# Kernel optimization log

Measured on AMD Instinct MI355X. Metric: run time of the kernel, lower is better.

## Reference

```python
import jax, jax.numpy as jnp
import numpy as np

# --- hyperparameters (from MambaBlock init) ---
DIM = 256          # d_model per window
STEP = 128         # int(dim * hop), hop = 0.5
N_MAMBA = 2
D_STATE = 16
D_CONV = 4
EXPAND = 4
D_INNER = EXPAND * DIM          # 1024
DT_RANK = -(-DIM // 16)         # ceil(d_model/16) = 16
EPS = 1e-5
B_SZ = 4
T_LEN = 131072


def setup_inputs() -> dict:
    key = jax.random.key(0)
    ks = jax.random.split(key, 8)
    s = 0.02
    x = jax.random.normal(ks[0], (B_SZ, T_LEN), dtype=jnp.float32)
    in_proj_w = jax.random.normal(ks[1], (N_MAMBA, 2 * D_INNER, DIM), dtype=jnp.float32) * s
    conv_w = jax.random.normal(ks[2], (N_MAMBA, D_INNER, 1, D_CONV), dtype=jnp.float32) * 0.1
    conv_b = jnp.zeros((N_MAMBA, D_INNER), dtype=jnp.float32)
    x_proj_w = jax.random.normal(ks[3], (N_MAMBA, DT_RANK + 2 * D_STATE, D_INNER), dtype=jnp.float32) * s
    dt_std = DT_RANK ** -0.5
    dt_proj_w = jax.random.uniform(ks[4], (N_MAMBA, D_INNER, DT_RANK), minval=-dt_std, maxval=dt_std, dtype=jnp.float32)
    # dt bias: inverse-softplus of dt ~ LogUniform[1e-3, 0.1] (mamba_ssm init)
    dt = jnp.exp(jax.random.uniform(ks[5], (N_MAMBA, D_INNER), dtype=jnp.float32)
                 * (np.log(0.1) - np.log(1e-3)) + np.log(1e-3))
    dt_proj_b = dt + jnp.log(-jnp.expm1(-dt))
    A_log = jnp.log(jnp.broadcast_to(jnp.arange(1, D_STATE + 1, dtype=jnp.float32),
                                     (N_MAMBA, D_INNER, D_STATE)))
    D_param = jnp.ones((N_MAMBA, D_INNER), dtype=jnp.float32)
    out_proj_w = jax.random.normal(ks[6], (N_MAMBA, DIM, D_INNER), dtype=jnp.float32) * s
    norm_w = jnp.ones((N_MAMBA, DIM), dtype=jnp.float32)
    return dict(x=x, in_proj_w=in_proj_w, conv_w=conv_w, conv_b=conv_b,
                x_proj_w=x_proj_w, dt_proj_w=dt_proj_w, dt_proj_b=dt_proj_b,
                A_log=A_log, D_param=D_param, out_proj_w=out_proj_w, norm_w=norm_w)


def _rmsnorm(x, w):
    return x * jax.lax.rsqrt(jnp.mean(x * x, axis=-1, keepdims=True) + EPS) * w


def _selective_scan(u, delta, A, Bm, Cm, Dp):
    # u, delta: [B, L, Di]; A: [Di, N]; Bm, Cm: [B, L, N]; Dp: [Di]
    def step(h, inp):
        u_t, d_t, B_t, C_t = inp                       # [B,Di],[B,Di],[B,N],[B,N]
        dA = jnp.exp(d_t[:, :, None] * A)              # [B,Di,N]
        h = dA * h + (d_t * u_t)[:, :, None] * B_t[:, None, :]
        y_t = jnp.einsum('bdn,bn->bd', h, C_t)
        return h, y_t
    h0 = jnp.zeros((u.shape[0], u.shape[2], A.shape[1]), u.dtype)
    xs = (u.transpose(1, 0, 2), delta.transpose(1, 0, 2),
          Bm.transpose(1, 0, 2), Cm.transpose(1, 0, 2))
    _, ys = jax.lax.scan(step, h0, xs)                 # ys: [L, B, Di]
    return ys.transpose(1, 0, 2) + u * Dp


def _mamba(x, in_w, cw, cb, xp_w, dt_w, dt_b, A_log, Dp, out_w):
    # x: [B, L, d_model]
    xz = jnp.einsum('bld,ed->ble', x, in_w)            # [B, L, 2*Di]
    xc, z = jnp.split(xz, 2, axis=-1)
    # causal depthwise conv (torch pads d_conv-1 both sides then truncates to L)
    xc = xc.transpose(0, 2, 1)                         # [B, Di, L]
    xc = jax.lax.conv_general_dilated(xc, cw, window_strides=(1,),
                                      padding=[(D_CONV - 1, 0)],
                                      feature_group_count=D_INNER,
                                      dimension_numbers=('NCH', 'OIH', 'NCH'))
    xc = jax.nn.silu(xc + cb[None, :, None]).transpose(0, 2, 1)  # [B, L, Di]
    x_dbl = jnp.einsum('bld,ed->ble', xc, xp_w)        # [B, L, dt_rank + 2N]
    dt = x_dbl[..., :DT_RANK]
    Bm = x_dbl[..., DT_RANK:DT_RANK + D_STATE]
    Cm = x_dbl[..., DT_RANK + D_STATE:]
    delta = jax.nn.softplus(jnp.einsum('blr,dr->bld', dt, dt_w) + dt_b)
    A = -jnp.exp(A_log)                                # [Di, N]
    y = _selective_scan(xc, delta, A, Bm, Cm, Dp)
    y = y * jax.nn.silu(z)
    return jnp.einsum('bld,ed->ble', y, out_w)         # [B, L, d_model]


def _forward(x, in_proj_w, conv_w, conv_b, x_proj_w, dt_proj_w, dt_proj_b,
             A_log, D_param, out_proj_w, norm_w):
    B, T = x.shape
    L = (T - DIM) // STEP + 1
    idx = jnp.arange(L)[:, None] * STEP + jnp.arange(DIM)[None, :]  # [L, DIM]
    h = x[:, idx]                                      # unfold -> [B, L, DIM]
    res = None
    for i in range(N_MAMBA):
        res = h + res if res is not None else h        # Block residual chaining
        hn = _rmsnorm(res, norm_w[i])
        h = _mamba(hn, in_proj_w[i], conv_w[i], conv_b[i], x_proj_w[i],
                   dt_proj_w[i], dt_proj_b[i], A_log[i], D_param[i], out_proj_w[i])
    r = h + res
    # hop < 1: triangular window, then fold (overlap-add)
    half = DIM // 2
    win = jnp.concatenate([jnp.linspace(0.0, 1.0, half), jnp.linspace(1.0, 0.0, half)])
    r = r * win
    folded = jnp.zeros_like(x).at[:, idx].add(r)       # F.fold overlap-add
    return folded + x


def reference(x, in_proj_w, conv_w, conv_b, x_proj_w, dt_proj_w, dt_proj_b,
              A_log, D_param, out_proj_w, norm_w):
    return _forward(x, in_proj_w, conv_w, conv_b, x_proj_w, dt_proj_w, dt_proj_b,
                    A_log, D_param, out_proj_w, norm_w)
```

## Files before the change

kernel.cpp:

```cpp
#include <hip/hip_runtime.h>
#include <cmath>

#define DIMC   256
#define L_WIN  1023
#define M_VALID 4092
#define M_PAD  4096
#define DI     1024
#define TLEN   131072
#define SEG    64
#define NSEG   16
#define CBT    8

typedef __bf16 bf16x8 __attribute__((ext_vector_type(8)));
typedef __bf16 bf16x4 __attribute__((ext_vector_type(4)));
typedef float  f32x4  __attribute__((ext_vector_type(4)));

#define LOG2E 1.4426950408889634f

__device__ __forceinline__ float sigmoidf_(float x){ return 1.f/(1.f + __expf(-x)); }
__device__ __forceinline__ float softplusf_(float v){ return fmaxf(v,0.f) + log1pf(__expf(-fabsf(v))); }

template<int CTRL>
__device__ __forceinline__ float dpp_add(float x){
  int v = __builtin_amdgcn_update_dpp(0, __builtin_bit_cast(int, x), CTRL, 0xF, 0xF, true);
  return x + __builtin_bit_cast(float, v);
}

__global__ __launch_bounds__(256) void init_kernel(const float* __restrict__ x, float* __restrict__ res,
    __bf16* __restrict__ hn16, const float* __restrict__ w0,
    const float* __restrict__ a, __bf16* __restrict__ da, int na,
    const float* __restrict__ b, __bf16* __restrict__ db, int nb,
    const float* __restrict__ c, __bf16* __restrict__ dc, int nc)
{
  if (blockIdx.x < M_PAD){
    int m = blockIdx.x, j = threadIdx.x;
    float v = 0.f;
    if (m < M_VALID){
      int bb = m / L_WIN, l = m - bb*L_WIN;
      v = x[(size_t)bb*TLEN + l*128 + j];
    }
    res[(size_t)m*DIMC + j] = v;
    float s = v*v;
    #pragma unroll
    for (int off = 32; off; off >>= 1) s += __shfl_down(s, off);
    __shared__ float ls[4];
    if ((threadIdx.x & 63) == 0) ls[threadIdx.x >> 6] = s;
    __syncthreads();
    float tot = ls[0] + ls[1] + ls[2] + ls[3];
    float scale = rsqrtf(tot * (1.f/DIMC) + 1e-5f);
    hn16[(size_t)m*DIMC + j] = (__bf16)(v * scale * w0[j]);
    return;
  }
  int nblk = gridDim.x - M_PAD;
  int stride = nblk*256;
  int base = (blockIdx.x - M_PAD)*256 + threadIdx.x;
  for (int i = base; i < na; i += stride) da[i] = (__bf16)a[i];
  for (int i = base; i < nb; i += stride) db[i] = (__bf16)b[i];
  for (int i = base; i < nc; i += stride) dc[i] = (__bf16)c[i];
}

__global__ __launch_bounds__(256) void rms_kernel(const float* __restrict__ src, __bf16* __restrict__ dst,
                                                  const float* __restrict__ w){
  int m = blockIdx.x, j = threadIdx.x;
  float v = (m < M_VALID) ? src[(size_t)m*DIMC + j] : 0.f;
  float s = v*v;
  #pragma unroll
  for (int off = 32; off; off >>= 1) s += __shfl_down(s, off);
  __shared__ float ls[4];
  if ((threadIdx.x & 63) == 0) ls[threadIdx.x >> 6] = s;
  __syncthreads();
  float tot = ls[0] + ls[1] + ls[2] + ls[3];
  float scale = rsqrtf(tot * (1.f/DIMC) + 1e-5f);
  dst[(size_t)m*DIMC + j] = (__bf16)(v * scale * w[j]);
}

template<int WM, int WN, typename OutT>
__global__ __launch_bounds__(256) void gemm_tiled_kernel(const __bf16* __restrict__ A, const __bf16* __restrict__ B,
    OutT* C, const float* addsrc, int K, int ldc)
{
  constexpr int BM  = 32*WM;
  constexpr int BN  = 32*WN;
  constexpr int LDK = 72;
  __shared__ __bf16 As[BM*LDK];
  __shared__ __bf16 Bs[BN*LDK];
  int tid  = threadIdx.x;
  int lane = tid & 63, wv = tid >> 6;
  int row  = lane & 15, kq = lane >> 4;
  int m0 = blockIdx.x*BM, n0 = blockIdx.y*BN;
  int wmo = (wv >> 1)*(16*WM);
  int wno = (wv &  1)*(16*WN);
  f32x4 acc[WM][WN] = {};
  for (int kt = 0; kt < K; kt += 64){
    __syncthreads();
    #pragma unroll
    for (int r = 0; r < BM/32; ++r){
      int seg = r*256 + tid;
      int rw = seg >> 3, sb = seg & 7;
      *(bf16x8*)(As + rw*LDK + sb*8) = *(const bf16x8*)(A + (size_t)(m0 + rw)*K + kt + sb*8);
    }
    #pragma unroll
    for (int r = 0; r < BN/32; ++r){
      int seg = r*256 + tid;
      int rw = seg >> 3, sb = seg & 7;
      *(bf16x8*)(Bs + rw*LDK + sb*8) = *(const bf16x8*)(B + (size_t)(n0 + rw)*K + kt + sb*8);
    }
    __syncthreads();
    #pragma unroll
    for (int ks = 0; ks < 2; ++ks){
      bf16x8 af[WM], bfr[WN];
      #pragma unroll
      for (int i = 0; i < WM; ++i) af[i]  = *(const bf16x8*)(As + (wmo + i*16 + row)*LDK + ks*32 + kq*8);
      #pragma unroll
      for (int j = 0; j < WN; ++j) bfr[j] = *(const bf16x8*)(Bs + (wno + j*16 + row)*LDK + ks*32 + kq*8);
      #pragma unroll
      for (int i = 0; i < WM; ++i){
        #pragma unroll
        for (int j = 0; j < WN; ++j)
          acc[i][j] = __builtin_amdgcn_mfma_f32_16x16x32_bf16(af[i], bfr[j], acc[i][j], 0, 0, 0);
      }
    }
  }
  #pragma unroll
  for (int i = 0; i < WM; ++i){
    int cm = m0 + wmo + i*16 + kq*4;
    #pragma unroll
    for (int j = 0; j < WN; ++j){
      int cn = n0 + wno + j*16 + row;
      #pragma unroll
      for (int ii = 0; ii < 4; ++ii){
        size_t idx = (size_t)(cm + ii)*ldc + cn;
        float v = acc[i][j][ii];
        if (addsrc) v += addsrc[idx];
        C[idx] = (OutT)v;
      }
    }
  }
}

__global__ __launch_bounds__(256) void conv_xproj_dt_kernel(
  const __bf16* __restrict__ xz16, const float* __restrict__ cw, const float* __restrict__ cb,
  const __bf16* __restrict__ wxp, const float* __restrict__ dtw, const float* __restrict__ dtb,
  __bf16* __restrict__ u16, float* __restrict__ xdbl, __bf16* __restrict__ delta16)
{
  __shared__ __bf16 su[16][1032];
  __shared__ float  sdt[CBT][17];
  __shared__ f32x4  spart[4][3][64];
  int tid = threadIdx.x;
  int m0 = blockIdx.x * CBT;
  {
    int d = tid * 4;
    float w[4][4], bias[4];
    #pragma unroll
    for (int c = 0; c < 4; ++c){
      #pragma unroll
      for (int j = 0; j < 4; ++j) w[c][j] = cw[(d + c)*4 + j];
      bias[c] = cb[d + c];
    }
    bf16x4 zero4; zero4[0] = (__bf16)0.f; zero4[1] = (__bf16)0.f; zero4[2] = (__bf16)0.f; zero4[3] = (__bf16)0.f;
    bf16x4 rm3 = (m0 >= 3) ? *(const bf16x4*)(xz16 + (size_t)(m0-3)*2048 + d) : zero4;
    bf16x4 rm2 = (m0 >= 2) ? *(const bf16x4*)(xz16 + (size_t)(m0-2)*2048 + d) : zero4;
    bf16x4 rm1 = (m0 >= 1) ? *(const bf16x4*)(xz16 + (size_t)(m0-1)*2048 + d) : zero4;
    for (int ti = 0; ti < CBT; ++ti){
      int m = m0 + ti;
      bf16x4 cur = *(const bf16x4*)(xz16 + (size_t)m*2048 + d);
      float acc[4] = {0.f, 0.f, 0.f, 0.f};
      if (m < M_VALID){
        int b = m / L_WIN;
        int l = m - b*L_WIN;
        #pragma unroll
        for (int c = 0; c < 4; ++c) acc[c] = fmaf((float)cur[c], w[c][3], bias[c]);
        if (l >= 1){
          #pragma unroll
          for (int c = 0; c < 4; ++c) acc[c] = fmaf((float)rm1[c], w[c][2], acc[c]);
        }
        if (l >= 2){
          #pragma unroll
          for (int c = 0; c < 4; ++c) acc[c] = fmaf((float)rm2[c], w[c][1], acc[c]);
        }
        if (l >= 3){
          #pragma unroll
          for (int c = 0; c < 4; ++c) acc[c] = fmaf((float)rm3[c], w[c][0], acc[c]);
        }
        #pragma unroll
        for (int c = 0; c < 4; ++c) acc[c] = acc[c] * sigmoidf_(acc[c]);
      }
      bf16x4 o;
      #pragma unroll
      for (int c = 0; c < 4; ++c) o[c] = (__bf16)acc[c];
      *(bf16x4*)(u16 + (size_t)m*DI + d) = o;
      *(bf16x4*)(&su[ti][d]) = o;
      rm3 = rm2; rm2 = rm1; rm1 = cur;
    }
  }
  __syncthreads();
  {
    int lane = tid & 63, wv = tid >> 6;
    int row = lane & 15, kq = lane >> 4;
    int kbase = wv * 256;
    f32x4 acc0 = {0,0,0,0}, acc1 = {0,0,0,0}, acc2 = {0,0,0,0};
    const __bf16* B0 = wxp + (size_t)(row)*1024      + kbase + kq*8;
    const __bf16* B1 = wxp + (size_t)(16 + row)*1024 + kbase + kq*8;
    const __bf16* B2 = wxp + (size_t)(32 + row)*1024 + kbase + kq*8;
    #pragma unroll
    for (int k = 0; k < 256; k += 32){
      bf16x8 a = *(const bf16x8*)(&su[row][kbase + k + kq*8]);
      acc0 = __builtin_amdgcn_mfma_f32_16x16x32_bf16(a, *(const bf16x8*)(B0 + k), acc0, 0, 0, 0);
      acc1 = __builtin_amdgcn_mfma_f32_16x16x32_bf16(a, *(const bf16x8*)(B1 + k), acc1, 0, 0, 0);
      acc2 = __builtin_amdgcn_mfma_f32_16x16x32_bf16(a, *(const bf16x8*)(B2 + k), acc2, 0, 0, 0);
    }
    spart[wv][0][lane] = acc0;
    spart[wv][1][lane] = acc1;
    spart[wv][2][lane] = acc2;
  }
  __syncthreads();
  if (tid < 192){
    int tno = tid >> 6, lane = tid & 63;
    int row = lane & 15, kq = lane >> 4;
    f32x4 sum = spart[0][tno][lane];
    sum += spart[1][tno][lane];
    sum += spart[2][tno][lane];
    sum += spart[3][tno][lane];
    #pragma unroll
    for (int i = 0; i < 4; ++i){
      int tok = kq*4 + i;
      if (tok < CBT){
        xdbl[(size_t)(m0 + tok)*48 + tno*16 + row] = sum[i];
        if (tno == 0) sdt[tok][row] = sum[i];
      }
    }
  }
  __syncthreads();
  {
    int d0 = tid * 4;
    float w[4][16], bias[4];
    #pragma unroll
    for (int c = 0; c < 4; ++c){
      #pragma unroll
      for (int q = 0; q < 16; ++q) w[c][q] = dtw[(d0 + c)*16 + q];
      bias[c] = dtb[d0 + c];
    }
    for (int t = 0; t < CBT; ++t){
      float acc[4] = {bias[0], bias[1], bias[2], bias[3]};
      #pragma unroll
      for (int r = 0; r < 16; ++r){
        float dv = sdt[t][r];
        #pragma unroll
        for (int c = 0; c < 4; ++c) acc[c] = fmaf(dv, w[c][r], acc[c]);
      }
      bf16x4 o;
      #pragma unroll
      for (int c = 0; c < 4; ++c) o[c] = (__bf16)softplusf_(acc[c]);
      *(bf16x4*)(delta16 + (size_t)(m0 + t)*DI + d0) = o;
    }
  }
}

__global__ __launch_bounds__(256) void scan_part1_kernel(
  const __bf16* __restrict__ u16, const __bf16* __restrict__ delta16,
  const float* __restrict__ xdbl, const float* __restrict__ Alog, float2* __restrict__ Pq)
{
  int bid = blockIdx.x;
  int s = bid & 15, dtile = (bid >> 4) & 63, b = bid >> 10;
  if (s == 15) return;
  int d0 = dtile << 4;
  int tid = threadIdx.x;
  int c = tid >> 4, n = tid & 15;
  float A2 = -__expf(Alog[(d0 + c)*16 + n]) * LOG2E;
  __shared__ float2 sdd[16][SEG+2];
  __shared__ float  sB [SEG][17];
  int t0 = s*SEG;
  int nt = L_WIN - t0; if (nt > SEG) nt = SEG;
  size_t base_m = (size_t)b*L_WIN + t0;
  if (tid < 128){
    int row = tid >> 1, half = tid & 1;
    bf16x8 dl8, u8;
    if (row < nt){
      size_t m = base_m + row;
      dl8 = *(const bf16x8*)(delta16 + m*DI + d0 + half*8);
      u8  = *(const bf16x8*)(u16    + m*DI + d0 + half*8);
    } else {
      #pragma unroll
      for (int j = 0; j < 8; ++j){ dl8[j] = (__bf16)0.f; u8[j] = (__bf16)0.f; }
    }
    #pragma unroll
    for (int j = 0; j < 8; ++j){
      float dlt = (float)dl8[j];
      sdd[half*8 + j][row] = make_float2(dlt, dlt * (float)u8[j]);
    }
  }
  {
    int row = tid & 63, q = tid >> 6;
    f32x4 B4 = {0,0,0,0};
    if (row < nt) B4 = *(const f32x4*)(xdbl + (base_m + row)*48 + 16 + q*4);
    #pragma unroll
    for (int j = 0; j < 4; ++j) sB[row][q*4 + j] = B4[j];
  }
  __syncthreads();
  float h = 0.f, sd = 0.f;
  #pragma unroll 8
  for (int t = 0; t < SEG; ++t){
    float2 dd2 = sdd[c][t];
    float dA = exp2f(dd2.x * A2);
    h = fmaf(dA, h, dd2.y * sB[t][n]);
    sd += dd2.x;
  }
  float P = exp2f(sd * A2);
  Pq[(((size_t)b*NSEG + s) << 14) + (dtile << 8) + tid] = make_float2(P, h);
}

__global__ __launch_bounds__(256) void scan_part2_kernel(
  const __bf16* __restrict__ u16, const __bf16* __restrict__ delta16,
  const float* __restrict__ xdbl, const __bf16* __restrict__ xz16,
  const float* __restrict__ Alog, const float* __restrict__ Dp,
  const float2* __restrict__ Pq, __bf16* __restrict__ y16)
{
  int bid = blockIdx.x;
  int s = bid & 15, dtile = (bid >> 4) & 63, b = bid >> 10;
  int d0 = dtile << 4;
  int tid = threadIdx.x;
  int c = tid >> 4, n = tid & 15;
  float A2 = -__expf(Alog[(d0 + c)*16 + n]) * LOG2E;
  __shared__ float2 sdd[16][SEG+2];
  __shared__ float2 sBC[SEG][17];
  __shared__ float  sD[16];
  if (tid < 16) sD[tid] = Dp[d0 + tid];
  int t0 = s*SEG;
  int nt = L_WIN - t0; if (nt > SEG) nt = SEG;
  size_t base_m = (size_t)b*L_WIN + t0;
  if (tid < 128){
    int row = tid >> 1, half = tid & 1;
    bf16x8 dl8, u8;
    if (row < nt){
      size_t m = base_m + row;
      dl8 = *(const bf16x8*)(delta16 + m*DI + d0 + half*8);
      u8  = *(const bf16x8*)(u16    + m*DI + d0 + half*8);
    } else {
      #pragma unroll
      for (int j = 0; j < 8; ++j){ dl8[j] = (__bf16)0.f; u8[j] = (__bf16)0.f; }
    }
    #pragma unroll
    for (int j = 0; j < 8; ++j){
      float dlt = (float)dl8[j];
      sdd[half*8 + j][row] = make_float2(dlt, dlt * (float)u8[j]);
    }
  }
  {
    int row = tid & 63, q = tid >> 6;
    f32x4 B4 = {0,0,0,0}, C4 = {0,0,0,0};
    if (row < nt){
      size_t m = base_m + row;
      B4 = *(const f32x4*)(xdbl + m*48 + 16 + q*4);
      C4 = *(const f32x4*)(xdbl + m*48 + 32 + q*4);
    }
    #pragma unroll
    for (int j = 0; j < 4; ++j) sBC[row][q*4 + j] = make_float2(B4[j], C4[j]);
  }
  float h = 0.f;
  {
    size_t pqbase = (((size_t)b*NSEG) << 14) + (dtile << 8) + tid;
    for (int s0 = 0; s0 < 15; s0 += 8){
      if (s0 >= s) break;
      float2 r[8];
      #pragma unroll
      for (int j = 0; j < 8; ++j)
        r[j] = Pq[pqbase + ((size_t)(s0 + j) << 14)];
      #pragma unroll
      for (int j = 0; j < 8; ++j)
        if (s0 + j < s) h = fmaf(r[j].x, h, r[j].y);
    }
  }
  __syncthreads();
  bool wl = ((n & 7) == 0);
  int wslot = n >> 3;
  #pragma unroll 8
  for (int t = 0; t < SEG; ++t){
    float2 dd2 = sdd[c][t];
    float dA = exp2f(dd2.x * A2);
    float2 bc = sBC[t][n];
    h = fmaf(dA, h, dd2.y * bc.x);
    float pp = h * bc.y;
    pp = dpp_add<0xB1>(pp);
    pp = dpp_add<0x4E>(pp);
    pp = dpp_add<0x141>(pp);
    if (wl) ((float*)&sdd[c][t])[wslot] = pp;
  }
  __syncthreads();
  if (tid < 128){
    int tt = tid >> 1, half = tid & 1;
    if (tt < nt){
      size_t m = base_m + tt;
      bf16x8 z8 = *(const bf16x8*)(xz16 + m*2048 + 1024 + d0 + half*8);
      bf16x8 u8 = *(const bf16x8*)(u16 + m*DI + d0 + half*8);
      bf16x8 o;
      #pragma unroll
      for (int j = 0; j < 8; ++j){
        int dd = half*8 + j;
        float2 yh = sdd[dd][tt];
        float zv = (float)z8[j];
        float yv = ((yh.x + yh.y) + (float)u8[j] * sD[dd]) * (zv * sigmoidf_(zv));
        o[j] = (__bf16)yv;
      }
      *(bf16x8*)(y16 + m*DI + d0 + half*8) = o;
    }
  }
}

__global__ __launch_bounds__(256) void fold_kernel(const float* __restrict__ x, const float* __restrict__ r,
                                                   float* __restrict__ out){
  int i = blockIdx.x*256 + threadIdx.x;
  int b = i >> 17;
  int t = i & (TLEN - 1);
  float acc = x[i];
  int l1 = t >> 7;
  int j  = t & 127;
  if (l1 < L_WIN) acc += r[((size_t)b*L_WIN + l1)*DIMC + j] * ((float)j * (1.f/127.f));
  if (l1 >= 1)    acc += r[((size_t)b*L_WIN + l1 - 1)*DIMC + j + 128] * ((float)(127 - j) * (1.f/127.f));
  out[i] = acc;
}

extern "C" void kernel_launch(void* const* d_in, const int* in_sizes, int n_in,
                              void* d_out, int out_size, void* d_ws, size_t ws_size,
                              hipStream_t stream)
{
  (void)in_sizes; (void)n_in; (void)out_size; (void)ws_size;
  const float* x      = (const float*)d_in[0];
  const float* in_w   = (const float*)d_in[1];
  const float* conv_w = (const float*)d_in[2];
  const float* conv_b = (const float*)d_in[3];
  const float* xp_w   = (const float*)d_in[4];
  const float* dt_w   = (const float*)d_in[5];
  const float* dt_b   = (const float*)d_in[6];
  const float* A_log  = (const float*)d_in[7];
  const float* Dp     = (const float*)d_in[8];
  const float* out_w  = (const float*)d_in[9];
  const float* norm_w = (const float*)d_in[10];
  float* out = (float*)d_out;

  char* p = (char*)d_ws;
  auto alloc = [&](size_t bytes)->void*{ void* r = (void*)p; p += (bytes + 255) & ~(size_t)255; return r; };
  float*  res    = (float*) alloc((size_t)M_PAD*DIMC*4);
  __bf16* hn16   = (__bf16*)alloc((size_t)M_PAD*DIMC*2);
  __bf16* xz16   = (__bf16*)alloc((size_t)M_PAD*2048*2);
  __bf16* u16    = (__bf16*)alloc((size_t)M_PAD*DI*2);
  float*  xdbl   = (float*) alloc((size_t)M_PAD*48*4);
  __bf16* delta16= (__bf16*)alloc((size_t)M_PAD*DI*2);
  __bf16* y16    = (__bf16*)alloc((size_t)M_PAD*DI*2);
  float2* Pq     = (float2*)alloc((size_t)4*NSEG*16384*8);
  __bf16* w_in16 = (__bf16*)alloc((size_t)2*2048*256*2);
  __bf16* w_xp16 = (__bf16*)alloc((size_t)2*48*1024*2);
  __bf16* w_out16= (__bf16*)alloc((size_t)2*256*1024*2);

  init_kernel<<<M_PAD + 512, 256, 0, stream>>>(x, res, hn16, norm_w,
                                               in_w, w_in16, 2*2048*256,
                                               xp_w, w_xp16, 2*48*1024,
                                               out_w, w_out16, 2*256*1024);

  for (int i = 0; i < 2; ++i){
    if (i == 1)
      rms_kernel<<<M_PAD, 256, 0, stream>>>(res, hn16, norm_w + 256);
    gemm_tiled_kernel<4, 2, __bf16><<<dim3(32, 32), 256, 0, stream>>>(hn16, w_in16 + (size_t)i*524288, xz16, nullptr, 256, 2048);
    conv_xproj_dt_kernel<<<M_PAD/CBT, 256, 0, stream>>>(xz16, conv_w + i*4096, conv_b + i*1024,
                                                        w_xp16 + (size_t)i*49152, dt_w + i*16384, dt_b + i*1024,
                                                        u16, xdbl, delta16);
    scan_part1_kernel<<<4096, 256, 0, stream>>>(u16, delta16, xdbl, A_log + i*16384, Pq);
    scan_part2_kernel<<<4096, 256, 0, stream>>>(u16, delta16, xdbl, xz16, A_log + i*16384, Dp + i*1024,
                                                Pq, y16);
    gemm_tiled_kernel<1, 1, float><<<dim3(128, 8), 256, 0, stream>>>(y16, w_out16 + (size_t)i*262144, res, res, 1024, 256);
  }
  fold_kernel<<<TLEN*4/256, 256, 0, stream>>>(x, res, out);
}
```

Before: 299.0 us.

## Fuse second-layer RMSNorm into out-proj epilogue and in-proj prologue; transpose scan smem

Removes the separate rms_kernel. The first out-projection GEMM epilogue now accumulates per-row sums of squares with DPP reductions and atomics, and a new in-projection GEMM normalizes the raw fp32 residual while loading its A tile. The selective-scan kernels also transpose their B/C shared-memory layout so each thread can read two timesteps at once with vector loads. The cost is atomic contention and fp32 A-tile loads redone across 32 column blocks, in exchange for one fewer launch and less intermediate traffic.

Measured after the change: 296.2 us. About the same (-1.0%).

```diff
diff --git a/kernel.cpp b/kernel.cpp
--- a/kernel.cpp
+++ b/kernel.cpp
@@ -27,7 +27,7 @@
 }
 
 __global__ __launch_bounds__(256) void init_kernel(const float* __restrict__ x, float* __restrict__ res,
-    __bf16* __restrict__ hn16, const float* __restrict__ w0,
+    __bf16* __restrict__ hn16, const float* __restrict__ w0, float* __restrict__ rowsum,
     const float* __restrict__ a, __bf16* __restrict__ da, int na,
     const float* __restrict__ b, __bf16* __restrict__ db, int nb,
     const float* __restrict__ c, __bf16* __restrict__ dc, int nc)
@@ -54,29 +54,15 @@
   int nblk = gridDim.x - M_PAD;
   int stride = nblk*256;
   int base = (blockIdx.x - M_PAD)*256 + threadIdx.x;
+  for (int i = base; i < M_PAD; i += stride) rowsum[i] = 0.f;
   for (int i = base; i < na; i += stride) da[i] = (__bf16)a[i];
   for (int i = base; i < nb; i += stride) db[i] = (__bf16)b[i];
   for (int i = base; i < nc; i += stride) dc[i] = (__bf16)c[i];
 }
 
-__global__ __launch_bounds__(256) void rms_kernel(const float* __restrict__ src, __bf16* __restrict__ dst,
-                                                  const float* __restrict__ w){
-  int m = blockIdx.x, j = threadIdx.x;
-  float v = (m < M_VALID) ? src[(size_t)m*DIMC + j] : 0.f;
-  float s = v*v;
-  #pragma unroll
-  for (int off = 32; off; off >>= 1) s += __shfl_down(s, off);
-  __shared__ float ls[4];
-  if ((threadIdx.x & 63) == 0) ls[threadIdx.x >> 6] = s;
-  __syncthreads();
-  float tot = ls[0] + ls[1] + ls[2] + ls[3];
-  float scale = rsqrtf(tot * (1.f/DIMC) + 1e-5f);
-  dst[(size_t)m*DIMC + j] = (__bf16)(v * scale * w[j]);
-}
-
 template<int WM, int WN, typename OutT>
 __global__ __launch_bounds__(256) void gemm_tiled_kernel(const __bf16* __restrict__ A, const __bf16* __restrict__ B,
-    OutT* C, const float* addsrc, int K, int ldc)
+    OutT* C, const float* addsrc, float* rowsum_out, int K, int ldc)
 {
   constexpr int BM  = 32*WM;
   constexpr int BN  = 32*WN;
@@ -124,15 +110,102 @@
   for (int i = 0; i < WM; ++i){
     int cm = m0 + wmo + i*16 + kq*4;
     #pragma unroll
-    for (int j = 0; j < WN; ++j){
-      int cn = n0 + wno + j*16 + row;
-      #pragma unroll
-      for (int ii = 0; ii < 4; ++ii){
+    for (int ii = 0; ii < 4; ++ii){
+      float sq = 0.f;
+      #pragma unroll
+      for (int j = 0; j < WN; ++j){
+        int cn = n0 + wno + j*16 + row;
         size_t idx = (size_t)(cm + ii)*ldc + cn;
         float v = acc[i][j][ii];
         if (addsrc) v += addsrc[idx];
         C[idx] = (OutT)v;
-      }
+        sq += v*v;
+      }
+      if (rowsum_out){
+        sq = dpp_add<0xB1>(sq);
+        sq = dpp_add<0x4E>(sq);
+        sq = dpp_add<0x141>(sq);
+        sq = dpp_add<0x128>(sq);
+        if (row == 0) atomicAdd(rowsum_out + cm + ii, sq);
+      }
+    }
+  }
+}
+
+__global__ __launch_bounds__(256) void gemm_rms2_kernel(const float* __restrict__ Araw,
+    const __bf16* __restrict__ B, const float* __restrict__ rowsum, const float* __restrict__ wn,
+    __bf16* __restrict__ C, int ldc)
+{
+  constexpr int WM = 4, WN = 2;
+  constexpr int BM = 128, BN = 64, LDK = 72;
+  __shared__ __bf16 As[BM*LDK];
+  __shared__ __bf16 Bs[BN*LDK];
+  __shared__ float  sscale[BM];
+  __shared__ float  swn[256];
+  int tid  = threadIdx.x;
+  int lane = tid & 63, wv = tid >> 6;
+  int row  = lane & 15, kq = lane >> 4;
+  int m0 = blockIdx.x*BM, n0 = blockIdx.y*BN;
+  int wmo = (wv >> 1)*(16*WM);
+  int wno = (wv &  1)*(16*WN);
+  swn[tid] = wn[tid];
+  if (tid < BM){
+    int gr = m0 + tid;
+    sscale[tid] = (gr < M_VALID) ? rsqrtf(rowsum[gr]*(1.f/DIMC) + 1e-5f) : 0.f;
+  }
+  f32x4 acc[WM][WN] = {};
+  for (int kt = 0; kt < 256; kt += 64){
+    __syncthreads();
+    #pragma unroll
+    for (int r2 = 0; r2 < BM/32; ++r2){
+      int seg = r2*256 + tid;
+      int rw = seg >> 3, sb = seg & 7;
+      int gr = m0 + rw;
+      float sc = sscale[rw];
+      f32x4 v0 = {0,0,0,0}, v1 = {0,0,0,0};
+      if (gr < M_VALID){
+        const float* ap = Araw + (size_t)gr*DIMC + kt + sb*8;
+        v0 = *(const f32x4*)ap; v1 = *(const f32x4*)(ap + 4);
+      }
+      bf16x8 o;
+      #pragma unroll
+      for (int j = 0; j < 4; ++j){
+        o[j]   = (__bf16)(v0[j] * sc * swn[kt + sb*8 + j]);
+        o[4+j] = (__bf16)(v1[j] * sc * swn[kt + sb*8 + 4 + j]);
+      }
+      *(bf16x8*)(As + rw*LDK + sb*8) = o;
+    }
+    #pragma unroll
+    for (int r2 = 0; r2 < BN/32; ++r2){
+      int seg = r2*256 + tid;
+      int rw = seg >> 3, sb = seg & 7;
+      *(bf16x8*)(Bs + rw*LDK + sb*8) = *(const bf16x8*)(B + (size_t)(n0 + rw)*256 + kt + sb*8);
+    }
+    __syncthreads();
+    #pragma unroll
+    for (int ks = 0; ks < 2; ++ks){
+      bf16x8 af[WM], bfr[WN];
+      #pragma unroll
+      for (int i = 0; i < WM; ++i) af[i]  = *(const bf16x8*)(As + (wmo + i*16 + row)*LDK + ks*32 + kq*8);
+      #pragma unroll
+      for (int j = 0; j < WN; ++j) bfr[j] = *(const bf16x8*)(Bs + (wno + j*16 + row)*LDK + ks*32 + kq*8);
+      #pragma unroll
+      for (int i = 0; i < WM; ++i){
+        #pragma unroll
+        for (int j = 0; j < WN; ++j)
+          acc[i][j] = __builtin_amdgcn_mfma_f32_16x16x32_bf16(af[i], bfr[j], acc[i][j], 0, 0, 0);
+      }
+    }
+  }
+  #pragma unroll
+  for (int i = 0; i < WM; ++i){
+    int cm = m0 + wmo + i*16 + kq*4;
+    #pragma unroll
+    for (int j = 0; j < WN; ++j){
+      int cn = n0 + wno + j*16 + row;
+      #pragma unroll
+      for (int ii = 0; ii < 4; ++ii)
+        C[(size_t)(cm + ii)*ldc + cn] = (__bf16)acc[i][j][ii];
     }
   }
 }
@@ -267,7 +340,7 @@
   int c = tid >> 4, n = tid & 15;
   float A2 = -__expf(Alog[(d0 + c)*16 + n]) * LOG2E;
   __shared__ float2 sdd[16][SEG+2];
-  __shared__ float  sB [SEG][17];
+  __shared__ float  sBt[16][SEG+2];
   int t0 = s*SEG;
   int nt = L_WIN - t0; if (nt > SEG) nt = SEG;
   size_t base_m = (size_t)b*L_WIN + t0;
@@ -293,16 +366,20 @@
     f32x4 B4 = {0,0,0,0};
     if (row < nt) B4 = *(const f32x4*)(xdbl + (base_m + row)*48 + 16 + q*4);
     #pragma unroll
-    for (int j = 0; j < 4; ++j) sB[row][q*4 + j] = B4[j];
+    for (int j = 0; j < 4; ++j) sBt[q*4 + j][row] = B4[j];
   }
   __syncthreads();
   float h = 0.f, sd = 0.f;
-  #pragma unroll 8
-  for (int t = 0; t < SEG; ++t){
-    float2 dd2 = sdd[c][t];
-    float dA = exp2f(dd2.x * A2);
-    h = fmaf(dA, h, dd2.y * sB[t][n]);
-    sd += dd2.x;
+  #pragma unroll 4
+  for (int t = 0; t < SEG; t += 2){
+    f32x4 dp  = *(const f32x4*)&sdd[c][t];
+    float2 b2 = *(const float2*)&sBt[n][t];
+    float dA0 = exp2f(dp[0] * A2);
+    h = fmaf(dA0, h, dp[1] * b2.x);
+    sd += dp[0];
+    float dA1 = exp2f(dp[2] * A2);
+    h = fmaf(dA1, h, dp[3] * b2.y);
+    sd += dp[2];
   }
   float P = exp2f(sd * A2);
   Pq[(((size_t)b*NSEG + s) << 14) + (dtile << 8) + tid] = make_float2(P, h);
@@ -320,8 +397,8 @@
   int tid = threadIdx.x;
   int c = tid >> 4, n = tid & 15;
   float A2 = -__expf(Alog[(d0 + c)*16 + n]) * LOG2E;
-  __shared__ float2 sdd[16][SEG+2];
-  __shared__ float2 sBC[SEG][17];
+  __shared__ float2 sdd [16][SEG+2];
+  __shared__ float2 sBCt[16][SEG+2];
   __shared__ float  sD[16];
   if (tid < 16) sD[tid] = Dp[d0 + tid];
   int t0 = s*SEG;
@@ -353,7 +430,7 @@
       C4 = *(const f32x4*)(xdbl + m*48 + 32 + q*4);
     }
     #pragma unroll
-    for (int j = 0; j < 4; ++j) sBC[row][q*4 + j] = make_float2(B4[j], C4[j]);
+    for (int j = 0; j < 4; ++j) sBCt[q*4 + j][row] = make_float2(B4[j], C4[j]);
   }
   float h = 0.f;
   {
@@ -372,17 +449,24 @@
   __syncthreads();
   bool wl = ((n & 7) == 0);
   int wslot = n >> 3;
-  #pragma unroll 8
-  for (int t = 0; t < SEG; ++t){
-    float2 dd2 = sdd[c][t];
-    float dA = exp2f(dd2.x * A2);
-    float2 bc = sBC[t][n];
-    h = fmaf(dA, h, dd2.y * bc.x);
-    float pp = h * bc.y;
-    pp = dpp_add<0xB1>(pp);
-    pp = dpp_add<0x4E>(pp);
-    pp = dpp_add<0x141>(pp);
-    if (wl) ((float*)&sdd[c][t])[wslot] = pp;
+  #pragma unroll 4
+  for (int t = 0; t < SEG; t += 2){
+    f32x4 dp = *(const f32x4*)&sdd[c][t];
+    f32x4 bc = *(const f32x4*)&sBCt[n][t];
+    float dA0 = exp2f(dp[0] * A2);
+    h = fmaf(dA0, h, dp[1] * bc[0]);
+    float pp0 = h * bc[1];
+    pp0 = dpp_add<0xB1>(pp0);
+    pp0 = dpp_add<0x4E>(pp0);
+    pp0 = dpp_add<0x141>(pp0);
+    if (wl) ((float*)&sdd[c][t])[wslot] = pp0;
+    float dA1 = exp2f(dp[2] * A2);
+    h = fmaf(dA1, h, dp[3] * bc[2]);
+    float pp1 = h * bc[3];
+    pp1 = dpp_add<0xB1>(pp1);
+    pp1 = dpp_add<0x4E>(pp1);
+    pp1 = dpp_add<0x141>(pp1);
+    if (wl) ((float*)&sdd[c][t+1])[wslot] = pp1;
   }
   __syncthreads();
   if (tid < 128){
@@ -446,26 +530,29 @@
   __bf16* delta16= (__bf16*)alloc((size_t)M_PAD*DI*2);
   __bf16* y16    = (__bf16*)alloc((size_t)M_PAD*DI*2);
   float2* Pq     = (float2*)alloc((size_t)4*NSEG*16384*8);
+  float*  rowsum = (float*) alloc((size_t)M_PAD*4);
   __bf16* w_in16 = (__bf16*)alloc((size_t)2*2048*256*2);
   __bf16* w_xp16 = (__bf16*)alloc((size_t)2*48*1024*2);
   __bf16* w_out16= (__bf16*)alloc((size_t)2*256*1024*2);
 
-  init_kernel<<<M_PAD + 512, 256, 0, stream>>>(x, res, hn16, norm_w,
+  init_kernel<<<M_PAD + 512, 256, 0, stream>>>(x, res, hn16, norm_w, rowsum,
                                                in_w, w_in16, 2*2048*256,
                                                xp_w, w_xp16, 2*48*1024,
                                                out_w, w_out16, 2*256*1024);
 
   for (int i = 0; i < 2; ++i){
-    if (i == 1)
-      rms_kernel<<<M_PAD, 256, 0, stream>>>(res, hn16, norm_w + 256);
-    gemm_tiled_kernel<4, 2, __bf16><<<dim3(32, 32), 256, 0, stream>>>(hn16, w_in16 + (size_t)i*524288, xz16, nullptr, 256, 2048);
+    if (i == 0)
+      gemm_tiled_kernel<4, 2, __bf16><<<dim3(32, 32), 256, 0, stream>>>(hn16, w_in16, xz16, nullptr, nullptr, 256, 2048);
+    else
+      gemm_rms2_kernel<<<dim3(32, 32), 256, 0, stream>>>(res, w_in16 + 524288, rowsum, norm_w + 256, xz16, 2048);
     conv_xproj_dt_kernel<<<M_PAD/CBT, 256, 0, stream>>>(xz16, conv_w + i*4096, conv_b + i*1024,
                                                         w_xp16 + (size_t)i*49152, dt_w + i*16384, dt_b + i*1024,
                                                         u16, xdbl, delta16);
     scan_part1_kernel<<<4096, 256, 0, stream>>>(u16, delta16, xdbl, A_log + i*16384, Pq);
     scan_part2_kernel<<<4096, 256, 0, stream>>>(u16, delta16, xdbl, xz16, A_log + i*16384, Dp + i*1024,
                                                 Pq, y16);
-    gemm_tiled_kernel<1, 1, float><<<dim3(128, 8), 256, 0, stream>>>(y16, w_out16 + (size_t)i*262144, res, res, 1024, 256);
+    gemm_tiled_kernel<1, 1, float><<<dim3(128, 8), 256, 0, stream>>>(y16, w_out16 + (size_t)i*262144, res, res,
+                                                                     (i == 0) ? rowsum : nullptr, 1024, 256);
   }
   fold_kernel<<<TLEN*4/256, 256, 0, stream>>>(x, res, out);
 }
```
